# Performance work log

Measured on AMD Instinct MI355X. Metric: run time of the kernel, lower is better.

The kernel has to match this reference:

```python
import jax, jax.numpy as jnp
import numpy as np

B, L, DM = 2, 1024, 1024
DI = 2 * DM          # expand=2
N = 16               # d_state
K = 4                # d_conv
DTR = DM // 16       # dt_rank = ceil(d_model/16) = 64
EPS = 1e-5


def setup_inputs() -> dict:
    key = jax.random.key(0)
    ks = jax.random.split(key, 8)
    s = lambda k, shape, sc=0.02: jax.random.normal(k, shape, jnp.float32) * sc
    return {
        "x": jax.random.normal(ks[0], (B, L, DM), jnp.float32),
        "ln_g": jnp.ones((DM,), jnp.float32),
        "ln_b": jnp.zeros((DM,), jnp.float32),
        "in_proj_w": s(ks[1], (2 * DI, DM)),
        "conv_w": s(ks[2], (DI, 1, K), 0.1),
        "conv_b": jnp.zeros((DI,), jnp.float32),
        "x_proj_w": s(ks[3], (DTR + 2 * N, DI)),
        "dt_proj_w": s(ks[4], (DI, DTR), 0.1),
        "dt_proj_b": s(ks[5], (DI,), 0.5),
        "A_log": jnp.log(jnp.tile(jnp.arange(1, N + 1, dtype=jnp.float32), (DI, 1))),
        "D": jnp.ones((DI,), jnp.float32),
        "out_proj_w": s(ks[6], (DM, DI)),
    }


def reference(x, ln_g, ln_b, in_proj_w, conv_w, conv_b, x_proj_w,
              dt_proj_w, dt_proj_b, A_log, D, out_proj_w):
    residual = x
    # LayerNorm
    mu = x.mean(-1, keepdims=True)
    var = ((x - mu) ** 2).mean(-1, keepdims=True)
    xn = (x - mu) * jax.lax.rsqrt(var + EPS) * ln_g + ln_b
    # in_proj -> (x, z)
    xz = jnp.einsum('bld,ed->ble', xn, in_proj_w)   # (B,L,2*DI)
    xi, z = jnp.split(xz, 2, axis=-1)
    # depthwise causal conv1d + SiLU
    xc = jax.lax.conv_general_dilated(
        xi.transpose(0, 2, 1), conv_w, (1,), [(K - 1, 0)],
        feature_group_count=DI, dimension_numbers=('NCH', 'OIH', 'NCH'))
    u = jax.nn.silu((xc + conv_b[None, :, None]).transpose(0, 2, 1))  # (B,L,DI)
    # x_proj -> dt, B, C
    xdbl = jnp.einsum('bld,ed->ble', u, x_proj_w)
    dt, Bc, Cc = jnp.split(xdbl, [DTR, DTR + N], axis=-1)
    delta = jax.nn.softplus(jnp.einsum('blr,dr->bld', dt, dt_proj_w) + dt_proj_b)
    A = -jnp.exp(A_log)                              # (DI,N)
    dA = jnp.exp(delta[..., None] * A)               # (B,L,DI,N)
    dBu = delta[..., None] * Bc[:, :, None, :] * u[..., None]

    def step(h, inp):
        dA_t, dBu_t, C_t = inp                        # (B,DI,N),(B,DI,N),(B,N)
        h = dA_t * h + dBu_t
        y = jnp.einsum('bdn,bn->bd', h, C_t)
        return h, y

    h0 = jnp.zeros((B, DI, N), x.dtype)
    _, ys = jax.lax.scan(step, h0, (dA.transpose(1, 0, 2, 3),
                                    dBu.transpose(1, 0, 2, 3),
                                    Cc.transpose(1, 0, 2)))
    y = ys.transpose(1, 0, 2) + u * D                # (B,L,DI)
    y = y * jax.nn.silu(z)
    out = jnp.einsum('bld,ed->ble', y, out_proj_w)
    return residual + out
```

## Files before the change

### kernel.cpp

```cpp
#include <hip/hip_runtime.h>
#include <hip/hip_bf16.h>
#include <math.h>

#define B_   2
#define L_   1024
#define DM_  1024
#define DI_  2048
#define NS_  16
#define DTR_ 64
#define M_   (B_ * L_)
#define XZW_ (2 * DI_)
#define XDW_ 128
#define CH_  32
#define CLEN_ (L_ / CH_)
#define SK_  8
#define KCH_ (DI_ / SK_)

typedef __attribute__((ext_vector_type(8))) short bf16x8;
typedef __attribute__((ext_vector_type(4))) float f32x4;
typedef __attribute__((ext_vector_type(4))) unsigned short u16x4;

static __device__ __forceinline__ unsigned short f2bf(float f) {
  __hip_bfloat16 h = __float2bfloat16(f);
  return *reinterpret_cast<unsigned short*>(&h);
}
static __device__ __forceinline__ float bf2f(unsigned short u) {
  unsigned int x = ((unsigned int)u) << 16;
  float f;
  __builtin_memcpy(&f, &x, 4);
  return f;
}

__global__ __launch_bounds__(256) void ln_kernel(
    const float* __restrict__ x, const float* __restrict__ g,
    const float* __restrict__ b, unsigned short* __restrict__ xnb)
{
  int r = blockIdx.x;
  int t = threadIdx.x;
  const float4* xr = (const float4*)(x + (size_t)r * DM_);
  float4 v = xr[t];
  float s  = v.x + v.y + v.z + v.w;
  float ss = v.x * v.x + v.y * v.y + v.z * v.z + v.w * v.w;
  for (int m = 32; m >= 1; m >>= 1) {
    s  += __shfl_down(s, m);
    ss += __shfl_down(ss, m);
  }
  __shared__ float sb[4], ssb[4];
  int w = t >> 6, lane = t & 63;
  if (lane == 0) { sb[w] = s; ssb[w] = ss; }
  __syncthreads();
  s  = sb[0] + sb[1] + sb[2] + sb[3];
  ss = ssb[0] + ssb[1] + ssb[2] + ssb[3];
  float mu  = s * (1.f / DM_);
  float var = ss * (1.f / DM_) - mu * mu;
  float rs  = rsqrtf(var + 1e-5f);
  float4 gv = ((const float4*)g)[t];
  float4 bv = ((const float4*)b)[t];
  u16x4 o;
  o[0] = f2bf((v.x - mu) * rs * gv.x + bv.x);
  o[1] = f2bf((v.y - mu) * rs * gv.y + bv.y);
  o[2] = f2bf((v.z - mu) * rs * gv.z + bv.z);
  o[3] = f2bf((v.w - mu) * rs * gv.w + bv.w);
  ((u16x4*)xnb)[r * 256 + t] = o;
}

__global__ __launch_bounds__(256) void f2bf_kernel(
    const float4* __restrict__ in, u16x4* __restrict__ outp)
{
  int i = blockIdx.x * 256 + threadIdx.x;
  float4 v = in[i];
  u16x4 o;
  o[0] = f2bf(v.x); o[1] = f2bf(v.y); o[2] = f2bf(v.z); o[3] = f2bf(v.w);
  outp[i] = o;
}

template<int MODE, int TN>
__global__ __launch_bounds__(256) void gemm_mfma(
    const short* __restrict__ A, int lda,
    const short* __restrict__ Bw, int ldb,
    void* __restrict__ Cv, int ldc, int Kdim,
    const float* __restrict__ res, int ldres,
    const float* __restrict__ bias)
{
  constexpr int MREP = (TN == 128) ? 4 : 2;
  constexpr int NREP = 4;
  constexpr int WM   = (TN == 128) ? 64 : 32;
  __shared__ __align__(16) short As[2][128 * 64];
  __shared__ __align__(16) short Bs[2][TN * 64];
  const int bm = blockIdx.y * 128, bn = blockIdx.x * TN;
  const int t = threadIdx.x, wid = t >> 6, lane = t & 63;
  const int wr = (TN == 128) ? (wid >> 1) : wid;
  const int wc = (TN == 128) ? (wid & 1) : 0;

  f32x4 acc[MREP][NREP];
#pragma unroll
  for (int i = 0; i < MREP; ++i)
#pragma unroll
    for (int j = 0; j < NREP; ++j) acc[i][j] = (f32x4){0.f, 0.f, 0.f, 0.f};

  const int srow = wid * 8 + (lane >> 3);
  const int sc   = lane & 7;
  const int r16 = lane & 15, khalf = lane >> 4;

  auto STAGE = [&](int buf, int k0) {
#pragma unroll
    for (int q = 0; q < 4; ++q) {
      int row = q * 32 + srow;
      int csw = sc ^ (row & 7);
      const short* gA = A + (size_t)(bm + row) * lda + k0 + csw * 8;
      __builtin_amdgcn_global_load_lds(
          (const __attribute__((address_space(1))) void*)gA,
          (__attribute__((address_space(3))) void*)(&As[buf][q * 2048 + wid * 512]),
          16, 0, 0);
    }
#pragma unroll
    for (int q = 0; q < TN / 32; ++q) {
      int row = q * 32 + srow;
      int csw = sc ^ (row & 7);
      const short* gB = Bw + (size_t)(bn + row) * ldb + k0 + csw * 8;
      __builtin_amdgcn_global_load_lds(
          (const __attribute__((address_space(1))) void*)gB,
          (__attribute__((address_space(3))) void*)(&Bs[buf][q * 2048 + wid * 512]),
          16, 0, 0);
    }
  };

  const int nt = Kdim >> 6;
  STAGE(0, 0);
  int cur = 0;
  for (int ti = 0; ti < nt; ++ti) {
    __syncthreads();
    if (ti + 1 < nt) STAGE(cur ^ 1, (ti + 1) << 6);

    bf16x8 af[MREP][2], bfr[NREP][2];
#pragma unroll
    for (int m = 0; m < MREP; ++m)
#pragma unroll
      for (int kk = 0; kk < 2; ++kk) {
        int c16 = kk * 4 + khalf;
        int rowa = wr * WM + m * 16 + r16;
        af[m][kk] = *(const bf16x8*)(&As[cur][rowa * 64 + ((c16 ^ (rowa & 7)) << 3)]);
      }
#pragma unroll
    for (int nn = 0; nn < NREP; ++nn)
#pragma unroll
      for (int kk = 0; kk < 2; ++kk) {
        int c16 = kk * 4 + khalf;
        int rowb = wc * 64 + nn * 16 + r16;
        bfr[nn][kk] = *(const bf16x8*)(&Bs[cur][rowb * 64 + ((c16 ^ (rowb & 7)) << 3)]);
      }
#pragma unroll
    for (int kk = 0; kk < 2; ++kk)
#pragma unroll
      for (int m = 0; m < MREP; ++m)
#pragma unroll
        for (int nn = 0; nn < NREP; ++nn)
          acc[m][nn] = __builtin_amdgcn_mfma_f32_16x16x32_bf16(
              af[m][kk], bfr[nn][kk], acc[m][nn], 0, 0, 0);
    cur ^= 1;
  }

  const int rgrp = lane >> 4;
#pragma unroll
  for (int m = 0; m < MREP; ++m)
#pragma unroll
    for (int nn = 0; nn < NREP; ++nn) {
      int col = bn + wc * 64 + nn * 16 + r16;
#pragma unroll
      for (int rg = 0; rg < 4; ++rg) {
        int row = bm + wr * WM + m * 16 + rgrp * 4 + rg;
        float v = acc[m][nn][rg];
        if (MODE == 1) {
          v += bias[col];
          v = (v > 20.f) ? v : log1pf(expf(v));
        }
        if (MODE == 2) v += res[(size_t)row * ldres + col];
        if (MODE == 3)
          ((unsigned short*)Cv)[(size_t)row * ldc + col] = f2bf(v);
        else
          ((float*)Cv)[(size_t)row * ldc + col] = v;
      }
    }
}

#define BM 64
#define BN 64
#define BK 32
#define PADR 68

__global__ __launch_bounds__(256) void gemm_nt_sk(
    const float* __restrict__ A, int lda,
    const float* __restrict__ Bw, int ldb,
    float* __restrict__ part, int Ncols)
{
  __shared__ float as[BK][PADR];
  __shared__ float bs[BK][PADR];
  int bm = blockIdx.y * BM;
  int bn = blockIdx.x * BN;
  int sk = blockIdx.z;
  int t  = threadIdx.x;
  int tx = t & 15, ty = t >> 4;

  float acc[4][4] = {};

  int m0 = t >> 3;
  int kq = t & 7;
  const float4 z4 = {0.f, 0.f, 0.f, 0.f};

  for (int k0 = sk * KCH_; k0 < (sk + 1) * KCH_; k0 += BK) {
    float4 a0 = *(const float4*)(A + (size_t)(bm + m0) * lda + k0 + kq * 4);
    float4 a1 = *(const float4*)(A + (size_t)(bm + m0 + 32) * lda + k0 + kq * 4);
    float4 b0 = (bn + m0 < Ncols)
        ? *(const float4*)(Bw + (size_t)(bn + m0) * ldb + k0 + kq * 4) : z4;
    float4 b1 = (bn + m0 + 32 < Ncols)
        ? *(const float4*)(Bw + (size_t)(bn + m0 + 32) * ldb + k0 + kq * 4) : z4;
    as[kq * 4 + 0][m0] = a0.x;  as[kq * 4 + 1][m0] = a0.y;
    as[kq * 4 + 2][m0] = a0.z;  as[kq * 4 + 3][m0] = a0.w;
    as[kq * 4 + 0][m0 + 32] = a1.x;  as[kq * 4 + 1][m0 + 32] = a1.y;
    as[kq * 4 + 2][m0 + 32] = a1.z;  as[kq * 4 + 3][m0 + 32] = a1.w;
    bs[kq * 4 + 0][m0] = b0.x;  bs[kq * 4 + 1][m0] = b0.y;
    bs[kq * 4 + 2][m0] = b0.z;  bs[kq * 4 + 3][m0] = b0.w;
    bs[kq * 4 + 0][m0 + 32] = b1.x;  bs[kq * 4 + 1][m0 + 32] = b1.y;
    bs[kq * 4 + 2][m0 + 32] = b1.z;  bs[kq * 4 + 3][m0 + 32] = b1.w;
    __syncthreads();

#pragma unroll
    for (int kk = 0; kk < BK; ++kk) {
      float4 a4 = *(const float4*)&as[kk][ty * 4];
      float4 b4 = *(const float4*)&bs[kk][tx * 4];
      float ar[4] = {a4.x, a4.y, a4.z, a4.w};
      float br[4] = {b4.x, b4.y, b4.z, b4.w};
#pragma unroll
      for (int i = 0; i < 4; ++i)
#pragma unroll
        for (int j = 0; j < 4; ++j)
          acc[i][j] = fmaf(ar[i], br[j], acc[i][j]);
    }
    __syncthreads();
  }

  float* outp = part + (size_t)sk * M_ * XDW_;
#pragma unroll
  for (int i = 0; i < 4; ++i) {
    int r = bm + ty * 4 + i;
    int c = bn + tx * 4;
    float4 o = {acc[i][0], acc[i][1], acc[i][2], acc[i][3]};
    *(float4*)(outp + (size_t)r * XDW_ + c) = o;
  }
}

__global__ __launch_bounds__(256) void reduce_sk(
    const float* __restrict__ part, float* __restrict__ xdbl,
    unsigned short* __restrict__ xdtb)
{
  int i = blockIdx.x * 256 + threadIdx.x;
  float s = 0.f;
#pragma unroll
  for (int sk = 0; sk < SK_; ++sk) s += part[(size_t)sk * M_ * XDW_ + i];
  xdbl[i] = s;
  int col = i & (XDW_ - 1);
  if (col < DTR_) xdtb[(size_t)(i >> 7) * DTR_ + col] = f2bf(s);
}

#define LCH 8
__global__ __launch_bounds__(256) void conv_silu_kernel(
    const unsigned short* __restrict__ xzb, const float* __restrict__ cw,
    const float* __restrict__ cb, float* __restrict__ u)
{
  int d  = blockIdx.x * 256 + threadIdx.x;
  int l0 = blockIdx.y * LCH;
  int b  = blockIdx.z;
  float w0 = cw[d * 4 + 0], w1 = cw[d * 4 + 1];
  float w2 = cw[d * 4 + 2], w3 = cw[d * 4 + 3];
  float bias = cb[d];
  const unsigned short* xi = xzb + (size_t)(b * L_) * XZW_ + d;
  float x3 = (l0 >= 3) ? bf2f(xi[(size_t)(l0 - 3) * XZW_]) : 0.f;
  float x2 = (l0 >= 2) ? bf2f(xi[(size_t)(l0 - 2) * XZW_]) : 0.f;
  float x1 = (l0 >= 1) ? bf2f(xi[(size_t)(l0 - 1) * XZW_]) : 0.f;
#pragma unroll
  for (int l = l0; l < l0 + LCH; ++l) {
    float x0 = bf2f(xi[(size_t)l * XZW_]);
    float v = w0 * x3 + w1 * x2 + w2 * x1 + w3 * x0 + bias;
    float uu = v / (1.f + __expf(-v));
    u[((size_t)(b * L_) + l) * DI_ + d] = uu;
    x3 = x2; x2 = x1; x1 = x0;
  }
}

__global__ __launch_bounds__(256) void scan_p1(
    const float* __restrict__ dlt, const float* __restrict__ u,
    const float* __restrict__ xdbl, const float* __restrict__ A_log,
    float* __restrict__ Pbuf, unsigned short* __restrict__ hend)
{
  int t = threadIdx.x;
  int ng = t & 3, dl = t >> 2;
  int d = blockIdx.x * 64 + dl;
  int b = blockIdx.y;
  int c = blockIdx.z;
  int l0 = c * CLEN_;
  float4 Al = *(const float4*)(A_log + d * NS_ + ng * 4);
  float A0 = -__expf(Al.x), A1 = -__expf(Al.y), A2 = -__expf(Al.z), A3 = -__expf(Al.w);
  float h0 = 0.f, h1 = 0.f, h2 = 0.f, h3 = 0.f, S = 0.f;
  const float* dp = dlt + ((size_t)(b * L_) + l0) * DI_ + d;
  const float* up = u   + ((size_t)(b * L_) + l0) * DI_ + d;
  const float* xp = xdbl + ((size_t)(b * L_) + l0) * XDW_ + DTR_ + ng * 4;
  float dv = dp[0], uv = up[0];
  float4 Bv = *(const float4*)xp;
  for (int l = 0; l < CLEN_; ++l) {
    int ln = (l + 1 < CLEN_) ? l + 1 : l;
    float dv_n = dp[(size_t)ln * DI_];
    float uv_n = up[(size_t)ln * DI_];
    float4 Bv_n = *(const float4*)(xp + (size_t)ln * XDW_);
    float dvu = dv * uv;
    h0 = __expf(dv * A0) * h0 + dvu * Bv.x;
    h1 = __expf(dv * A1) * h1 + dvu * Bv.y;
    h2 = __expf(dv * A2) * h2 + dvu * Bv.z;
    h3 = __expf(dv * A3) * h3 + dvu * Bv.w;
    S += dv;
    dv = dv_n; uv = uv_n; Bv = Bv_n;
  }
  size_t i = ((size_t)((b * CH_ + c) * DI_) + d) * NS_ + ng * 4;
  float4 P; P.x = __expf(S * A0); P.y = __expf(S * A1);
  P.z = __expf(S * A2); P.w = __expf(S * A3);
  u16x4 H; H[0] = f2bf(h0); H[1] = f2bf(h1); H[2] = f2bf(h2); H[3] = f2bf(h3);
  *(float4*)(Pbuf + i) = P;
  *(u16x4*)(hend + i) = H;
}

__global__ __launch_bounds__(256) void scan_p2(
    float* __restrict__ Pbuf, const unsigned short* __restrict__ hend)
{
  int tid = blockIdx.x * 256 + threadIdx.x;
  int n = tid & 15;
  int d = (tid >> 4) & (DI_ - 1);
  int b = tid >> 15;
  float h = 0.f;
  for (int c = 0; c < CH_; ++c) {
    size_t i = ((size_t)((b * CH_ + c) * DI_) + d) * NS_ + n;
    float Pv = Pbuf[i];
    float he = bf2f(hend[i]);
    Pbuf[i] = h;
    h = Pv * h + he;
  }
}

__global__ __launch_bounds__(256) void scan_p3(
    const float* __restrict__ dlt, const float* __restrict__ u,
    const float* __restrict__ xdbl, const float* __restrict__ A_log,
    const float* __restrict__ hin, const unsigned short* __restrict__ xzb,
    const float* __restrict__ Dp, unsigned short* __restrict__ yb)
{
  int t = threadIdx.x;
  int ng = t & 3, dl = t >> 2;
  int d = blockIdx.x * 64 + dl;
  int b = blockIdx.y;
  int c = blockIdx.z;
  int l0 = c * CLEN_;
  float4 Al = *(const float4*)(A_log + d * NS_ + ng * 4);
  float A0 = -__expf(Al.x), A1 = -__expf(Al.y), A2 = -__expf(Al.z), A3 = -__expf(Al.w);
  size_t i0 = ((size_t)((b * CH_ + c) * DI_) + d) * NS_ + ng * 4;
  float4 hv = *(const float4*)(hin + i0);
  float h0 = hv.x, h1 = hv.y, h2 = hv.z, h3 = hv.w;
  float Dd = Dp[d];
  const float* dp = dlt + ((size_t)(b * L_) + l0) * DI_ + d;
  const float* up = u   + ((size_t)(b * L_) + l0) * DI_ + d;
  const float* xp = xdbl + ((size_t)(b * L_) + l0) * XDW_ + DTR_ + ng * 4;
  const unsigned short* zp = xzb + ((size_t)(b * L_) + l0) * XZW_ + DI_ + d;
  unsigned short* yp = yb + ((size_t)(b * L_) + l0) * DI_ + d;
  float dv = dp[0], uv = up[0];
  float4 Bv = *(const float4*)xp;
  float4 Cv = *(const float4*)(xp + NS_);
  for (int l = 0; l < CLEN_; ++l) {
    int ln = (l + 1 < CLEN_) ? l + 1 : l;
    float dv_n = dp[(size_t)ln * DI_];
    float uv_n = up[(size_t)ln * DI_];
    float4 Bv_n = *(const float4*)(xp + (size_t)ln * XDW_);
    float4 Cv_n = *(const float4*)(xp + (size_t)ln * XDW_ + NS_);
    float dvu = dv * uv;
    h0 = __expf(dv * A0) * h0 + dvu * Bv.x;
    h1 = __expf(dv * A1) * h1 + dvu * Bv.y;
    h2 = __expf(dv * A2) * h2 + dvu * Bv.z;
    h3 = __expf(dv * A3) * h3 + dvu * Bv.w;
    float py = h0 * Cv.x + h1 * Cv.y + h2 * Cv.z + h3 * Cv.w;
    py += __shfl_xor(py, 1);
    py += __shfl_xor(py, 2);
    if (ng == 0) {
      float z = bf2f(zp[(size_t)l * XZW_]);
      float zs = z / (1.f + __expf(-z));
      yp[(size_t)l * DI_] = f2bf((py + uv * Dd) * zs);
    }
    dv = dv_n; uv = uv_n; Bv = Bv_n; Cv = Cv_n;
  }
}

extern "C" void kernel_launch(void* const* d_in, const int* in_sizes, int n_in,
                              void* d_out, int out_size, void* d_ws, size_t ws_size,
                              hipStream_t stream)
{
  const float* x         = (const float*)d_in[0];
  const float* ln_g      = (const float*)d_in[1];
  const float* ln_b      = (const float*)d_in[2];
  const float* in_proj_w = (const float*)d_in[3];
  const float* conv_w    = (const float*)d_in[4];
  const float* conv_b    = (const float*)d_in[5];
  const float* x_proj_w  = (const float*)d_in[6];
  const float* dt_proj_w = (const float*)d_in[7];
  const float* dt_proj_b = (const float*)d_in[8];
  const float* A_log     = (const float*)d_in[9];
  const float* Dp        = (const float*)d_in[10];
  const float* out_proj_w= (const float*)d_in[11];
  float* out = (float*)d_out;

  float* ws = (float*)d_ws;
  unsigned short* xzb = (unsigned short*)ws;
  float* u    = ws + 4194304;
  float* xdbl = ws + 8388608;
  float* dlt  = ws + 8650752;
  unsigned short* xdtb = (unsigned short*)(ws + 12845056);
  unsigned short* dtwb = (unsigned short*)(ws + 12910592);
  unsigned short* xnb  = (unsigned short*)(ws + 12976128);
  float* winb_f = ws + 14024704;
  unsigned short* winb  = (unsigned short*)winb_f;
  unsigned short* woutb = (unsigned short*)(ws + 16121856);
  unsigned short* yb    = (unsigned short*)(ws + 17170432);
  float* Pbuf = winb_f;
  unsigned short* hendb = xnb;

  ln_kernel<<<M_, 256, 0, stream>>>(x, ln_g, ln_b, xnb);

  f2bf_kernel<<<4096, 256, 0, stream>>>((const float4*)in_proj_w, (u16x4*)winb);
  f2bf_kernel<<<2048, 256, 0, stream>>>((const float4*)out_proj_w, (u16x4*)woutb);
  f2bf_kernel<<<128, 256, 0, stream>>>((const float4*)dt_proj_w, (u16x4*)dtwb);

  gemm_mfma<3, 128><<<dim3(XZW_ / 128, M_ / 128), 256, 0, stream>>>(
      (const short*)xnb, DM_, (const short*)winb, DM_, xzb, XZW_, DM_,
      nullptr, 0, nullptr);

  conv_silu_kernel<<<dim3(DI_ / 256, L_ / LCH, B_), 256, 0, stream>>>(
      xzb, conv_w, conv_b, u);

  gemm_nt_sk<<<dim3(XDW_ / BN, M_ / BM, SK_), 256, 0, stream>>>(
      u, DI_, x_proj_w, DI_, winb_f, 96);
  reduce_sk<<<(M_ * XDW_) / 256, 256, 0, stream>>>(winb_f, xdbl, xdtb);

  gemm_mfma<1, 128><<<dim3(DI_ / 128, M_ / 128), 256, 0, stream>>>(
      (const short*)xdtb, DTR_, (const short*)dtwb, DTR_, dlt, DI_, DTR_,
      nullptr, 0, dt_proj_b);

  scan_p1<<<dim3(DI_ / 64, B_, CH_), 256, 0, stream>>>(dlt, u, xdbl, A_log, Pbuf, hendb);
  scan_p2<<<(B_ * DI_ * NS_) / 256, 256, 0, stream>>>(Pbuf, hendb);
  scan_p3<<<dim3(DI_ / 64, B_, CH_), 256, 0, stream>>>(
      dlt, u, xdbl, A_log, Pbuf, xzb, Dp, yb);

  gemm_mfma<2, 64><<<dim3(DM_ / 64, M_ / 128), 256, 0, stream>>>(
      (const short*)yb, DI_, (const short*)woutb, DI_, out, DM_, DI_, x, DM_, nullptr);
}
```

Before: 271.5 us.

## Store u and delta in bf16, merge weight casts, double scan chunks

The conv output u and the softplus delta are now stored as bf16 rather than fp32. This roughly halves the memory traffic for the x_proj GEMM and both scan passes. The three weight-cast kernels are merged into one launch, and the scan uses 64 chunks instead of 32 for more parallelism. The workspace layout is reorganised so the split-K partials and Pbuf get separate buffers. The cost is extra rounding error in u and delta, plus larger per-chunk state buffers for the scan.

```diff
diff --git a/kernel.cpp b/kernel.cpp
--- a/kernel.cpp
+++ b/kernel.cpp
@@ -11,7 +11,7 @@
 #define M_   (B_ * L_)
 #define XZW_ (2 * DI_)
 #define XDW_ 128
-#define CH_  32
+#define CH_  64
 #define CLEN_ (L_ / CH_)
 #define SK_  8
 #define KCH_ (DI_ / SK_)
@@ -64,14 +64,21 @@
   ((u16x4*)xnb)[r * 256 + t] = o;
 }
 
-__global__ __launch_bounds__(256) void f2bf_kernel(
-    const float4* __restrict__ in, u16x4* __restrict__ outp)
+__global__ __launch_bounds__(256) void f2bf3_kernel(
+    const float4* __restrict__ w1, u16x4* __restrict__ o1, int n1,
+    const float4* __restrict__ w2, u16x4* __restrict__ o2, int n2,
+    const float4* __restrict__ w3, u16x4* __restrict__ o3, int n3)
 {
   int i = blockIdx.x * 256 + threadIdx.x;
-  float4 v = in[i];
+  const float4* src; u16x4* dst; int j;
+  if (i < n1)            { src = w1; dst = o1; j = i; }
+  else if (i < n1 + n2)  { src = w2; dst = o2; j = i - n1; }
+  else if (i < n1 + n2 + n3) { src = w3; dst = o3; j = i - n1 - n2; }
+  else return;
+  float4 v = src[j];
   u16x4 o;
   o[0] = f2bf(v.x); o[1] = f2bf(v.y); o[2] = f2bf(v.z); o[3] = f2bf(v.w);
-  outp[i] = o;
+  dst[j] = o;
 }
 
 template<int MODE, int TN>
@@ -170,12 +177,12 @@
       for (int rg = 0; rg < 4; ++rg) {
         int row = bm + wr * WM + m * 16 + rgrp * 4 + rg;
         float v = acc[m][nn][rg];
-        if (MODE == 1) {
+        if (MODE == 2) v += res[(size_t)row * ldres + col];
+        if (MODE == 4) {
           v += bias[col];
           v = (v > 20.f) ? v : log1pf(expf(v));
         }
-        if (MODE == 2) v += res[(size_t)row * ldres + col];
-        if (MODE == 3)
+        if (MODE == 3 || MODE == 4)
           ((unsigned short*)Cv)[(size_t)row * ldc + col] = f2bf(v);
         else
           ((float*)Cv)[(size_t)row * ldc + col] = v;
@@ -189,7 +196,7 @@
 #define PADR 68
 
 __global__ __launch_bounds__(256) void gemm_nt_sk(
-    const float* __restrict__ A, int lda,
+    const unsigned short* __restrict__ A, int lda,
     const float* __restrict__ Bw, int ldb,
     float* __restrict__ part, int Ncols)
 {
@@ -208,16 +215,16 @@
   const float4 z4 = {0.f, 0.f, 0.f, 0.f};
 
   for (int k0 = sk * KCH_; k0 < (sk + 1) * KCH_; k0 += BK) {
-    float4 a0 = *(const float4*)(A + (size_t)(bm + m0) * lda + k0 + kq * 4);
-    float4 a1 = *(const float4*)(A + (size_t)(bm + m0 + 32) * lda + k0 + kq * 4);
+    u16x4 a0u = *(const u16x4*)(A + (size_t)(bm + m0) * lda + k0 + kq * 4);
+    u16x4 a1u = *(const u16x4*)(A + (size_t)(bm + m0 + 32) * lda + k0 + kq * 4);
     float4 b0 = (bn + m0 < Ncols)
         ? *(const float4*)(Bw + (size_t)(bn + m0) * ldb + k0 + kq * 4) : z4;
     float4 b1 = (bn + m0 + 32 < Ncols)
         ? *(const float4*)(Bw + (size_t)(bn + m0 + 32) * ldb + k0 + kq * 4) : z4;
-    as[kq * 4 + 0][m0] = a0.x;  as[kq * 4 + 1][m0] = a0.y;
-    as[kq * 4 + 2][m0] = a0.z;  as[kq * 4 + 3][m0] = a0.w;
-    as[kq * 4 + 0][m0 + 32] = a1.x;  as[kq * 4 + 1][m0 + 32] = a1.y;
-    as[kq * 4 + 2][m0 + 32] = a1.z;  as[kq * 4 + 3][m0 + 32] = a1.w;
+    as[kq * 4 + 0][m0] = bf2f(a0u[0]);  as[kq * 4 + 1][m0] = bf2f(a0u[1]);
+    as[kq * 4 + 2][m0] = bf2f(a0u[2]);  as[kq * 4 + 3][m0] = bf2f(a0u[3]);
+    as[kq * 4 + 0][m0 + 32] = bf2f(a1u[0]);  as[kq * 4 + 1][m0 + 32] = bf2f(a1u[1]);
+    as[kq * 4 + 2][m0 + 32] = bf2f(a1u[2]);  as[kq * 4 + 3][m0 + 32] = bf2f(a1u[3]);
     bs[kq * 4 + 0][m0] = b0.x;  bs[kq * 4 + 1][m0] = b0.y;
     bs[kq * 4 + 2][m0] = b0.z;  bs[kq * 4 + 3][m0] = b0.w;
     bs[kq * 4 + 0][m0 + 32] = b1.x;  bs[kq * 4 + 1][m0 + 32] = b1.y;
@@ -265,7 +272,7 @@
 #define LCH 8
 __global__ __launch_bounds__(256) void conv_silu_kernel(
     const unsigned short* __restrict__ xzb, const float* __restrict__ cw,
-    const float* __restrict__ cb, float* __restrict__ u)
+    const float* __restrict__ cb, unsigned short* __restrict__ ub)
 {
   int d  = blockIdx.x * 256 + threadIdx.x;
   int l0 = blockIdx.y * LCH;
@@ -282,13 +289,13 @@
     float x0 = bf2f(xi[(size_t)l * XZW_]);
     float v = w0 * x3 + w1 * x2 + w2 * x1 + w3 * x0 + bias;
     float uu = v / (1.f + __expf(-v));
-    u[((size_t)(b * L_) + l) * DI_ + d] = uu;
+    ub[((size_t)(b * L_) + l) * DI_ + d] = f2bf(uu);
     x3 = x2; x2 = x1; x1 = x0;
   }
 }
 
 __global__ __launch_bounds__(256) void scan_p1(
-    const float* __restrict__ dlt, const float* __restrict__ u,
+    const unsigned short* __restrict__ dltb, const unsigned short* __restrict__ ub,
     const float* __restrict__ xdbl, const float* __restrict__ A_log,
     float* __restrict__ Pbuf, unsigned short* __restrict__ hend)
 {
@@ -301,15 +308,15 @@
   float4 Al = *(const float4*)(A_log + d * NS_ + ng * 4);
   float A0 = -__expf(Al.x), A1 = -__expf(Al.y), A2 = -__expf(Al.z), A3 = -__expf(Al.w);
   float h0 = 0.f, h1 = 0.f, h2 = 0.f, h3 = 0.f, S = 0.f;
-  const float* dp = dlt + ((size_t)(b * L_) + l0) * DI_ + d;
-  const float* up = u   + ((size_t)(b * L_) + l0) * DI_ + d;
+  const unsigned short* dp = dltb + ((size_t)(b * L_) + l0) * DI_ + d;
+  const unsigned short* up = ub   + ((size_t)(b * L_) + l0) * DI_ + d;
   const float* xp = xdbl + ((size_t)(b * L_) + l0) * XDW_ + DTR_ + ng * 4;
-  float dv = dp[0], uv = up[0];
+  float dv = bf2f(dp[0]), uv = bf2f(up[0]);
   float4 Bv = *(const float4*)xp;
   for (int l = 0; l < CLEN_; ++l) {
     int ln = (l + 1 < CLEN_) ? l + 1 : l;
-    float dv_n = dp[(size_t)ln * DI_];
-    float uv_n = up[(size_t)ln * DI_];
+    float dv_n = bf2f(dp[(size_t)ln * DI_]);
+    float uv_n = bf2f(up[(size_t)ln * DI_]);
     float4 Bv_n = *(const float4*)(xp + (size_t)ln * XDW_);
     float dvu = dv * uv;
     h0 = __expf(dv * A0) * h0 + dvu * Bv.x;
@@ -345,7 +352,7 @@
 }
 
 __global__ __launch_bounds__(256) void scan_p3(
-    const float* __restrict__ dlt, const float* __restrict__ u,
+    const unsigned short* __restrict__ dltb, const unsigned short* __restrict__ ub,
     const float* __restrict__ xdbl, const float* __restrict__ A_log,
     const float* __restrict__ hin, const unsigned short* __restrict__ xzb,
     const float* __restrict__ Dp, unsigned short* __restrict__ yb)
@@ -362,18 +369,18 @@
   float4 hv = *(const float4*)(hin + i0);
   float h0 = hv.x, h1 = hv.y, h2 = hv.z, h3 = hv.w;
   float Dd = Dp[d];
-  const float* dp = dlt + ((size_t)(b * L_) + l0) * DI_ + d;
-  const float* up = u   + ((size_t)(b * L_) + l0) * DI_ + d;
+  const unsigned short* dp = dltb + ((size_t)(b * L_) + l0) * DI_ + d;
+  const unsigned short* up = ub   + ((size_t)(b * L_) + l0) * DI_ + d;
   const float* xp = xdbl + ((size_t)(b * L_) + l0) * XDW_ + DTR_ + ng * 4;
   const unsigned short* zp = xzb + ((size_t)(b * L_) + l0) * XZW_ + DI_ + d;
   unsigned short* yp = yb + ((size_t)(b * L_) + l0) * DI_ + d;
-  float dv = dp[0], uv = up[0];
+  float dv = bf2f(dp[0]), uv = bf2f(up[0]);
   float4 Bv = *(const float4*)xp;
   float4 Cv = *(const float4*)(xp + NS_);
   for (int l = 0; l < CLEN_; ++l) {
     int ln = (l + 1 < CLEN_) ? l + 1 : l;
-    float dv_n = dp[(size_t)ln * DI_];
-    float uv_n = up[(size_t)ln * DI_];
+    float dv_n = bf2f(dp[(size_t)ln * DI_]);
+    float uv_n = bf2f(up[(size_t)ln * DI_]);
     float4 Bv_n = *(const float4*)(xp + (size_t)ln * XDW_);
     float4 Cv_n = *(const float4*)(xp + (size_t)ln * XDW_ + NS_);
     float dvu = dv * uv;
@@ -412,45 +419,46 @@
   float* out = (float*)d_out;
 
   float* ws = (float*)d_ws;
-  unsigned short* xzb = (unsigned short*)ws;
-  float* u    = ws + 4194304;
-  float* xdbl = ws + 8388608;
-  float* dlt  = ws + 8650752;
-  unsigned short* xdtb = (unsigned short*)(ws + 12845056);
-  unsigned short* dtwb = (unsigned short*)(ws + 12910592);
-  unsigned short* xnb  = (unsigned short*)(ws + 12976128);
-  float* winb_f = ws + 14024704;
-  unsigned short* winb  = (unsigned short*)winb_f;
-  unsigned short* woutb = (unsigned short*)(ws + 16121856);
-  unsigned short* yb    = (unsigned short*)(ws + 17170432);
-  float* Pbuf = winb_f;
-  unsigned short* hendb = xnb;
+  unsigned short* xzb  = (unsigned short*)ws;
+  unsigned short* ub   = (unsigned short*)(ws + 4194304);
+  float* xdbl          = ws + 6291456;
+  unsigned short* dltb = (unsigned short*)(ws + 6553600);
+  unsigned short* xdtb = (unsigned short*)(ws + 8650752);
+  unsigned short* dtwb = (unsigned short*)(ws + 8716288);
+  unsigned short* xnb  = (unsigned short*)(ws + 8781824);
+  unsigned short* winb = (unsigned short*)(ws + 9830400);
+  unsigned short* woutb= (unsigned short*)(ws + 11927552);
+  unsigned short* yb   = (unsigned short*)(ws + 12976128);
+  float* skpart        = ws + 14024704;
+  float* Pbuf          = ws + 16121856;
+  unsigned short* hendb= (unsigned short*)(ws + 20316160);
 
   ln_kernel<<<M_, 256, 0, stream>>>(x, ln_g, ln_b, xnb);
 
-  f2bf_kernel<<<4096, 256, 0, stream>>>((const float4*)in_proj_w, (u16x4*)winb);
-  f2bf_kernel<<<2048, 256, 0, stream>>>((const float4*)out_proj_w, (u16x4*)woutb);
-  f2bf_kernel<<<128, 256, 0, stream>>>((const float4*)dt_proj_w, (u16x4*)dtwb);
+  f2bf3_kernel<<<(1048576 + 524288 + 32768 + 255) / 256, 256, 0, stream>>>(
+      (const float4*)in_proj_w, (u16x4*)winb, 1048576,
+      (const float4*)out_proj_w, (u16x4*)woutb, 524288,
+      (const float4*)dt_proj_w, (u16x4*)dtwb, 32768);
 
   gemm_mfma<3, 128><<<dim3(XZW_ / 128, M_ / 128), 256, 0, stream>>>(
       (const short*)xnb, DM_, (const short*)winb, DM_, xzb, XZW_, DM_,
       nullptr, 0, nullptr);
 
   conv_silu_kernel<<<dim3(DI_ / 256, L_ / LCH, B_), 256, 0, stream>>>(
-      xzb, conv_w, conv_b, u);
+      xzb, conv_w, conv_b, ub);
 
   gemm_nt_sk<<<dim3(XDW_ / BN, M_ / BM, SK_), 256, 0, stream>>>(
-      u, DI_, x_proj_w, DI_, winb_f, 96);
-  reduce_sk<<<(M_ * XDW_) / 256, 256, 0, stream>>>(winb_f, xdbl, xdtb);
-
-  gemm_mfma<1, 128><<<dim3(DI_ / 128, M_ / 128), 256, 0, stream>>>(
-      (const short*)xdtb, DTR_, (const short*)dtwb, DTR_, dlt, DI_, DTR_,
+      ub, DI_, x_proj_w, DI_, skpart, 96);
+  reduce_sk<<<(M_ * XDW_) / 256, 256, 0, stream>>>(skpart, xdbl, xdtb);
+
+  gemm_mfma<4, 128><<<dim3(DI_ / 128, M_ / 128), 256, 0, stream>>>(
+      (const short*)xdtb, DTR_, (const short*)dtwb, DTR_, dltb, DI_, DTR_,
       nullptr, 0, dt_proj_b);
 
-  scan_p1<<<dim3(DI_ / 64, B_, CH_), 256, 0, stream>>>(dlt, u, xdbl, A_log, Pbuf, hendb);
+  scan_p1<<<dim3(DI_ / 64, B_, CH_), 256, 0, stream>>>(dltb, ub, xdbl, A_log, Pbuf, hendb);
   scan_p2<<<(B_ * DI_ * NS_) / 256, 256, 0, stream>>>(Pbuf, hendb);
   scan_p3<<<dim3(DI_ / 64, B_, CH_), 256, 0, stream>>>(
-      dlt, u, xdbl, A_log, Pbuf, xzb, Dp, yb);
+      dltb, ub, xdbl, A_log, Pbuf, xzb, Dp, yb);
 
   gemm_mfma<2, 64><<<dim3(DM_ / 64, M_ / 128), 256, 0, stream>>>(
       (const short*)yb, DI_, (const short*)woutb, DI_, out, DM_, DI_, x, DM_, nullptr);
```

New measurement: 270.1 us. Within noise of the previous version (-0.5%).
